# Performance work log

Hardware: AMD Instinct MI355X
Metric: run time of the kernel (lower is better)

Reference implementation:

```python
import jax, jax.numpy as jnp
import numpy as np

N, D, E = 16384, 1024, 65536
HID, H1, NCLS = 512, 8, 2


def _glorot(key, shape):
    fan = shape[0] + shape[-1]
    return jax.random.normal(key, shape, jnp.float32) * np.sqrt(2.0 / fan)


def setup_inputs() -> dict:
    key = jax.random.key(0)
    ks = jax.random.split(key, 12)
    return {
        "x": jax.random.normal(ks[0], (N, D), jnp.float32),
        "edge_index": jax.random.randint(ks[1], (2, E), 0, N, dtype=jnp.int32),
        # layer 1: GATConv((-1,-1), 512, heads=8, concat=True)
        "W1_src": _glorot(ks[2], (D, H1 * HID)),
        "W1_dst": _glorot(ks[3], (D, H1 * HID)),
        "att1_src": _glorot(ks[4], (H1, HID)),
        "att1_dst": _glorot(ks[5], (H1, HID)),
        "b1": jnp.zeros((H1 * HID,), jnp.float32),
        # layer 2: GATConv((-1,-1), 2, heads=1, concat=False)
        "W2_src": _glorot(ks[6], (H1 * HID, NCLS)),
        "W2_dst": _glorot(ks[7], (H1 * HID, NCLS)),
        "att2_src": _glorot(ks[8], (1, NCLS)),
        "att2_dst": _glorot(ks[9], (1, NCLS)),
        "b2": jnp.zeros((NCLS,), jnp.float32),
    }


def gat_layer(x, src, dst, Ws, Wd, a_s, a_d, b, heads, ch, concat):
    n = x.shape[0]
    hs = (x @ Ws).reshape(n, heads, ch)  # source-transformed feats [N,H,C]
    hd = (x @ Wd).reshape(n, heads, ch)  # dest-transformed feats  [N,H,C]
    al_s = jnp.einsum("nhc,hc->nh", hs, a_s)  # [N,H]
    al_d = jnp.einsum("nhc,hc->nh", hd, a_d)
    logits = jax.nn.leaky_relu(al_s[src] + al_d[dst], 0.2)  # [E,H]
    # segment softmax over incoming edges of each destination node
    m = jax.ops.segment_max(logits, dst, num_segments=n)
    m = jnp.where(jnp.isfinite(m), m, 0.0)
    e = jnp.exp(logits - m[dst])
    denom = jax.ops.segment_sum(e, dst, num_segments=n)
    alpha = e / (denom[dst] + 1e-16)  # [E,H]
    msg = hs[src] * alpha[:, :, None]  # [E,H,C]
    out = jax.ops.segment_sum(msg, dst, num_segments=n)  # [N,H,C]
    out = out.reshape(n, heads * ch) if concat else out.mean(axis=1)
    return out + b


def reference(x, edge_index, W1_src, W1_dst, att1_src, att1_dst, b1,
              W2_src, W2_dst, att2_src, att2_dst, b2):
    n = x.shape[0]
    # PyG GATConv adds self-loops by default
    loops = jnp.arange(n, dtype=edge_index.dtype)
    src = jnp.concatenate([edge_index[0], loops])
    dst = jnp.concatenate([edge_index[1], loops])
    h = gat_layer(x, src, dst, W1_src, W1_dst, att1_src, att1_dst, b1,
                  H1, HID, concat=True)  # [N, 4096]
    out = gat_layer(h, src, dst, W2_src, W2_dst, att2_src, att2_dst, b2,
                    1, NCLS, concat=False)  # [N, 2]
    return out
```

## Files before the change

kernel.cpp:

```cpp
#include <hip/hip_runtime.h>
#include <cstdint>
#include <cstddef>

#define DEV __device__ __forceinline__

typedef __attribute__((ext_vector_type(8))) short bf16x8;
typedef __attribute__((ext_vector_type(4))) float f32x4;

constexpr int N_  = 16384;
constexpr int D_  = 1024;
constexpr int E_  = 65536;
constexpr int ET_ = E_ + N_;
constexpr int H_  = 8;
constexpr int C_  = 512;
constexpr int F_  = 4096;
constexpr int KSPLIT = 2;
constexpr int ZS4 = KSPLIT * 48;
constexpr int NVB = 2048;
constexpr int NMB = (N_ / 16) * KSPLIT;

DEV unsigned short f2bf(float f){
  unsigned u = __float_as_uint(f);
  unsigned r = u + 0x7FFFu + ((u >> 16) & 1u);
  return (unsigned short)(r >> 16);
}
DEV float lrelu(float x){ return x >= 0.f ? x : 0.2f * x; }
DEV float waveSum(float v){
  #pragma unroll
  for (int o = 32; o > 0; o >>= 1) v += __shfl_xor(v, o);
  return v;
}
DEV int eSRC(const int* ei, int e){ return e < E_ ? ei[e]      : e - E_; }
DEV int eDST(const int* ei, int e){ return e < E_ ? ei[E_ + e] : e - E_; }

__global__ __launch_bounds__(256) void prep(
    const float* __restrict__ W1s, const float* __restrict__ W1d,
    const float* __restrict__ a1s, const float* __restrict__ a1d,
    const float* __restrict__ W2s, const float* __restrict__ W2d,
    const float* __restrict__ a2d, const float* __restrict__ b1,
    unsigned short* __restrict__ Vb, float* __restrict__ cb){
  int t = threadIdx.x;
  int bx = blockIdx.x;
  if (bx < NVB){
    int id = bx * 4 + (t >> 6);
    int lane = t & 63;
    int d = id >> 3, h = id & 7;
    float a2d0 = a2d[0], a2d1 = a2d[1];
    float sa = 0.f, sb = 0.f, s0 = 0.f, s1 = 0.f, sd = 0.f;
    #pragma unroll
    for (int i = 0; i < C_ / 64; i++){
      int c = i * 64 + lane;
      int gc = h * C_ + c;
      float ws  = W1s[(size_t)d * F_ + gc];
      float wdv = W1d[(size_t)d * F_ + gc];
      sa += ws * a1s[gc]; sb += wdv * a1d[gc];
      float2 w2 = *reinterpret_cast<const float2*>(W2s + (size_t)gc * 2);
      float2 wx = *reinterpret_cast<const float2*>(W2d + (size_t)gc * 2);
      s0 += ws * w2.x; s1 += ws * w2.y;
      sd += ws * (wx.x * a2d0 + wx.y * a2d1);
    }
    sa = waveSum(sa); sb = waveSum(sb);
    s0 = waveSum(s0); s1 = waveSum(s1); sd = waveSum(sd);
    if (lane == 0){
      int kc = d >> 5, ks = (d >> 3) & 3, ii = d & 7;
      auto put = [&](int jj, float v){
        int tt = jj >> 4, j = jj & 15;
        Vb[((size_t)(tt * 32 + kc) * 64 + ks * 16 + j) * 8 + ii] = f2bf(v);
      };
      put(h, sa); put(8 + h, sb); put(16 + h, s0); put(24 + h, s1); put(32 + h, sd);
    }
  } else {
    __shared__ float red[3][4];
    int w = t >> 6, lane = t & 63;
    float a2d0 = a2d[0], a2d1 = a2d[1];
    float p0 = 0.f, p1 = 0.f, pd = 0.f;
    for (int k = t; k < F_; k += 256){
      float b = b1[k];
      float2 w2 = *reinterpret_cast<const float2*>(W2s + (size_t)k * 2);
      float2 wx = *reinterpret_cast<const float2*>(W2d + (size_t)k * 2);
      p0 += b * w2.x; p1 += b * w2.y; pd += b * (wx.x * a2d0 + wx.y * a2d1);
    }
    p0 = waveSum(p0); p1 = waveSum(p1); pd = waveSum(pd);
    if (lane == 0){ red[0][w] = p0; red[1][w] = p1; red[2][w] = pd; }
    __syncthreads();
    if (t == 0){
      cb[0] = red[0][0] + red[0][1] + red[0][2] + red[0][3];
      cb[1] = red[1][0] + red[1][1] + red[1][2] + red[1][3];
      cb[2] = red[2][0] + red[2][1] + red[2][2] + red[2][3];
    }
  }
}

__global__ __launch_bounds__(64) void node_mfma(const float* __restrict__ X,
                                                const unsigned short* __restrict__ Vb,
                                                float* __restrict__ Z4,
                                                uint4* __restrict__ zr, int n16){
  int bx = blockIdx.x;
  int lane = threadIdx.x;
  if (bx >= NMB){
    int i = (bx - NMB) * 64 + lane;
    if (i < n16){ uint4 z = {0u,0u,0u,0u}; zr[i] = z; }
    return;
  }
  int n0 = (bx >> 1) * 16;
  int kh = bx & 1;
  int row = lane & 15, ks = lane >> 4;
  f32x4 ac0 = {0.f,0.f,0.f,0.f}, ac1 = ac0, ac2 = ac0;
  const float* xp = X + (size_t)(n0 + row) * D_ + ks * 8;
  constexpr int KC = 32 / KSPLIT;
  #pragma unroll 2
  for (int kk = 0; kk < KC; kk++){
    int kc = kh * KC + kk;
    float4 xa = *reinterpret_cast<const float4*>(xp + kc * 32);
    float4 xb = *reinterpret_cast<const float4*>(xp + kc * 32 + 4);
    bf16x8 a;
    a[0] = (short)f2bf(xa.x); a[1] = (short)f2bf(xa.y);
    a[2] = (short)f2bf(xa.z); a[3] = (short)f2bf(xa.w);
    a[4] = (short)f2bf(xb.x); a[5] = (short)f2bf(xb.y);
    a[6] = (short)f2bf(xb.z); a[7] = (short)f2bf(xb.w);
    bf16x8 b0 = *reinterpret_cast<const bf16x8*>(&Vb[((size_t)( 0 + kc) * 64 + lane) * 8]);
    bf16x8 b1 = *reinterpret_cast<const bf16x8*>(&Vb[((size_t)(32 + kc) * 64 + lane) * 8]);
    bf16x8 b2 = *reinterpret_cast<const bf16x8*>(&Vb[((size_t)(64 + kc) * 64 + lane) * 8]);
    ac0 = __builtin_amdgcn_mfma_f32_16x16x32_bf16(a, b0, ac0, 0, 0, 0);
    ac1 = __builtin_amdgcn_mfma_f32_16x16x32_bf16(a, b1, ac1, 0, 0, 0);
    ac2 = __builtin_amdgcn_mfma_f32_16x16x32_bf16(a, b2, ac2, 0, 0, 0);
  }
  #pragma unroll
  for (int r = 0; r < 4; r++){
    int n = n0 + ks * 4 + r;
    float* zp = Z4 + (size_t)n * ZS4 + kh * 48;
    zp[ 0 + row] = ac0[r];
    zp[16 + row] = ac1[r];
    zp[32 + row] = ac2[r];
  }
}

__global__ void edge1(const int* __restrict__ ei, const float* __restrict__ Z4,
                      float* __restrict__ den1, float* __restrict__ a0,
                      float* __restrict__ a1, float* __restrict__ ad){
  int t = blockIdx.x * blockDim.x + threadIdx.x;
  if (t >= ET_ * H_) return;
  int e = t >> 3, h = t & 7;
  int s = eSRC(ei, e), d = eDST(ei, e);
  const float* zs = Z4 + (size_t)s * ZS4;
  const float* zd = Z4 + (size_t)d * ZS4;
  float zsh = 0.f, zdh = 0.f, z0 = 0.f, z1 = 0.f, zdd = 0.f;
  #pragma unroll
  for (int k = 0; k < KSPLIT; k++){
    int o = k * 48;
    zsh += zs[o + h];
    zdh += zd[o + 8 + h];
    z0  += zs[o + 16 + h];
    z1  += zs[o + 24 + h];
    zdd += zs[o + 32 + h];
  }
  float ev = expf(lrelu(zsh + zdh));
  int o = d * 8 + h;
  atomicAdd(&den1[o], ev);
  atomicAdd(&a0[o], ev * z0);
  atomicAdd(&a1[o], ev * z1);
  atomicAdd(&ad[o], ev * zdd);
}

__global__ void node_mid(const float* __restrict__ den1, const float* __restrict__ a0,
                         const float* __restrict__ a1, const float* __restrict__ ad,
                         const float* __restrict__ cb, const float* __restrict__ a2s,
                         float4* __restrict__ Pn){
  int n = blockIdx.x * blockDim.x + threadIdx.x;
  if (n >= N_) return;
  float v0 = 0.f, v1 = 0.f, vd = 0.f;
  #pragma unroll
  for (int h = 0; h < 8; h++){
    float inv = 1.f / (den1[n * 8 + h] + 1e-16f);
    v0 += a0[n * 8 + h] * inv;
    v1 += a1[n * 8 + h] * inv;
    vd += ad[n * 8 + h] * inv;
  }
  v0 += cb[0]; v1 += cb[1]; vd += cb[2];
  float4 r;
  r.x = v0 * a2s[0] + v1 * a2s[1];
  r.y = v0; r.z = v1;
  r.w = vd;
  Pn[n] = r;
}

__global__ void edge2(const int* __restrict__ ei, const float4* __restrict__ Pn,
                      float* __restrict__ den2, float* __restrict__ o0,
                      float* __restrict__ o1){
  int e = blockIdx.x * blockDim.x + threadIdx.x;
  if (e >= ET_) return;
  int s = eSRC(ei, e), d = eDST(ei, e);
  float4 ps = Pn[s];
  float ald = Pn[d].w;
  float ev = expf(lrelu(ps.x + ald));
  atomicAdd(&den2[d], ev);
  atomicAdd(&o0[d], ev * ps.y);
  atomicAdd(&o1[d], ev * ps.z);
}

__global__ void node_out(const float* __restrict__ den2, const float* __restrict__ o0,
                         const float* __restrict__ o1, const float* __restrict__ b2,
                         float* __restrict__ out){
  int n = blockIdx.x * blockDim.x + threadIdx.x;
  if (n >= N_) return;
  float inv = 1.f / (den2[n] + 1e-16f);
  out[2 * n]     = o0[n] * inv + b2[0];
  out[2 * n + 1] = o1[n] * inv + b2[1];
}

extern "C" void kernel_launch(void* const* d_in, const int* in_sizes, int n_in,
                              void* d_out, int out_size, void* d_ws, size_t ws_size,
                              hipStream_t stream){
  const float* x   = (const float*)d_in[0];
  const int*   ei  = (const int*)  d_in[1];
  const float* W1s = (const float*)d_in[2];
  const float* W1d = (const float*)d_in[3];
  const float* a1s = (const float*)d_in[4];
  const float* a1d = (const float*)d_in[5];
  const float* b1  = (const float*)d_in[6];
  const float* W2s = (const float*)d_in[7];
  const float* W2d = (const float*)d_in[8];
  const float* a2s = (const float*)d_in[9];
  const float* a2d = (const float*)d_in[10];
  const float* b2  = (const float*)d_in[11];
  float* out = (float*)d_out;

  char* p = (char*)d_ws;
  auto alloc = [&](size_t bytes) -> void* {
    void* r = (void*)p;
    p += (bytes + 255) & ~(size_t)255;
    return r;
  };
  float* Z4 = (float*)alloc((size_t)N_ * ZS4 * 4);
  float* den1  = (float*)alloc((size_t)N_ * H_ * 4);
  float* a0    = (float*)alloc((size_t)N_ * H_ * 4);
  float* a1    = (float*)alloc((size_t)N_ * H_ * 4);
  float* ad    = (float*)alloc((size_t)N_ * H_ * 4);
  float* den2  = (float*)alloc((size_t)N_ * 4);
  float* o0    = (float*)alloc((size_t)N_ * 4);
  float* o1    = (float*)alloc((size_t)N_ * 4);
  unsigned short* Vb = (unsigned short*)alloc((size_t)3 * 32 * 64 * 8 * 2);
  float* cb    = (float*)alloc(256);
  float4* Pn   = (float4*)alloc((size_t)N_ * 16);

  size_t zrBytes = (size_t)((char*)Vb - (char*)den1);
  int n16 = (int)(zrBytes / 16);
  int nzb = (n16 + 63) / 64;

  prep<<<dim3(NVB + 1), dim3(256), 0, stream>>>(W1s, W1d, a1s, a1d, W2s, W2d,
                                                a2d, b1, Vb, cb);
  node_mfma<<<dim3(NMB + nzb), dim3(64), 0, stream>>>(x, Vb, Z4, (uint4*)den1, n16);
  edge1<<<dim3(ET_ * H_ / 256), dim3(256), 0, stream>>>(ei, Z4, den1, a0, a1, ad);
  node_mid<<<dim3(N_ / 256), dim3(256), 0, stream>>>(den1, a0, a1, ad, cb, a2s, Pn);
  edge2<<<dim3(ET_ / 256), dim3(256), 0, stream>>>(ei, Pn, den2, o0, o1);
  node_out<<<dim3(N_ / 256), dim3(256), 0, stream>>>(den2, o0, o1, b2, out);
}
```

Before: 67.19 us.

## Reduce K-split in-block via LDS and interleave edge accumulators per node

The node projection kernel now runs both K halves as two waves in one block and sums them through shared memory, so Z holds a single 48-float row per node instead of two partial rows. The edge kernel then reads each value once rather than summing two partials. The four per-head accumulators (denominator and three weighted sums) are merged into one node-major array of 32 floats, so the atomics for a node land in nearby cache lines. The cost is a block-wide barrier and LDS traffic in the projection kernel, plus fewer, larger blocks.

```diff
diff --git a/kernel.cpp b/kernel.cpp
--- a/kernel.cpp
+++ b/kernel.cpp
@@ -14,10 +14,9 @@
 constexpr int H_  = 8;
 constexpr int C_  = 512;
 constexpr int F_  = 4096;
-constexpr int KSPLIT = 2;
-constexpr int ZS4 = KSPLIT * 48;
+constexpr int ZS_ = 48;
 constexpr int NVB = 2048;
-constexpr int NMB = (N_ / 16) * KSPLIT;
+constexpr int NMB = N_ / 16;
 
 DEV unsigned short f2bf(float f){
   unsigned u = __float_as_uint(f);
@@ -91,26 +90,26 @@
   }
 }
 
-__global__ __launch_bounds__(64) void node_mfma(const float* __restrict__ X,
-                                                const unsigned short* __restrict__ Vb,
-                                                float* __restrict__ Z4,
-                                                uint4* __restrict__ zr, int n16){
+__global__ __launch_bounds__(128) void node_mfma(const float* __restrict__ X,
+                                                 const unsigned short* __restrict__ Vb,
+                                                 float* __restrict__ Z,
+                                                 uint4* __restrict__ zr, int n16){
   int bx = blockIdx.x;
-  int lane = threadIdx.x;
+  int t = threadIdx.x;
   if (bx >= NMB){
-    int i = (bx - NMB) * 64 + lane;
+    int i = (bx - NMB) * 128 + t;
     if (i < n16){ uint4 z = {0u,0u,0u,0u}; zr[i] = z; }
     return;
   }
-  int n0 = (bx >> 1) * 16;
-  int kh = bx & 1;
+  __shared__ float sm[16][52];
+  int kh = t >> 6, lane = t & 63;
+  int n0 = bx * 16;
   int row = lane & 15, ks = lane >> 4;
   f32x4 ac0 = {0.f,0.f,0.f,0.f}, ac1 = ac0, ac2 = ac0;
   const float* xp = X + (size_t)(n0 + row) * D_ + ks * 8;
-  constexpr int KC = 32 / KSPLIT;
   #pragma unroll 2
-  for (int kk = 0; kk < KC; kk++){
-    int kc = kh * KC + kk;
+  for (int kk = 0; kk < 16; kk++){
+    int kc = kh * 16 + kk;
     float4 xa = *reinterpret_cast<const float4*>(xp + kc * 32);
     float4 xb = *reinterpret_cast<const float4*>(xp + kc * 32 + 4);
     bf16x8 a;
@@ -125,56 +124,55 @@
     ac1 = __builtin_amdgcn_mfma_f32_16x16x32_bf16(a, b1, ac1, 0, 0, 0);
     ac2 = __builtin_amdgcn_mfma_f32_16x16x32_bf16(a, b2, ac2, 0, 0, 0);
   }
-  #pragma unroll
-  for (int r = 0; r < 4; r++){
-    int n = n0 + ks * 4 + r;
-    float* zp = Z4 + (size_t)n * ZS4 + kh * 48;
-    zp[ 0 + row] = ac0[r];
-    zp[16 + row] = ac1[r];
-    zp[32 + row] = ac2[r];
-  }
-}
-
-__global__ void edge1(const int* __restrict__ ei, const float* __restrict__ Z4,
-                      float* __restrict__ den1, float* __restrict__ a0,
-                      float* __restrict__ a1, float* __restrict__ ad){
+  if (kh == 1){
+    #pragma unroll
+    for (int r = 0; r < 4; r++){
+      int nl = ks * 4 + r;
+      sm[nl][ 0 + row] = ac0[r];
+      sm[nl][16 + row] = ac1[r];
+      sm[nl][32 + row] = ac2[r];
+    }
+  }
+  __syncthreads();
+  if (kh == 0){
+    #pragma unroll
+    for (int r = 0; r < 4; r++){
+      int nl = ks * 4 + r;
+      float* zp = Z + (size_t)(n0 + nl) * ZS_;
+      zp[ 0 + row] = ac0[r] + sm[nl][ 0 + row];
+      zp[16 + row] = ac1[r] + sm[nl][16 + row];
+      zp[32 + row] = ac2[r] + sm[nl][32 + row];
+    }
+  }
+}
+
+__global__ void edge1(const int* __restrict__ ei, const float* __restrict__ Z,
+                      float* __restrict__ acc){
   int t = blockIdx.x * blockDim.x + threadIdx.x;
   if (t >= ET_ * H_) return;
   int e = t >> 3, h = t & 7;
   int s = eSRC(ei, e), d = eDST(ei, e);
-  const float* zs = Z4 + (size_t)s * ZS4;
-  const float* zd = Z4 + (size_t)d * ZS4;
-  float zsh = 0.f, zdh = 0.f, z0 = 0.f, z1 = 0.f, zdd = 0.f;
-  #pragma unroll
-  for (int k = 0; k < KSPLIT; k++){
-    int o = k * 48;
-    zsh += zs[o + h];
-    zdh += zd[o + 8 + h];
-    z0  += zs[o + 16 + h];
-    z1  += zs[o + 24 + h];
-    zdd += zs[o + 32 + h];
-  }
-  float ev = expf(lrelu(zsh + zdh));
-  int o = d * 8 + h;
-  atomicAdd(&den1[o], ev);
-  atomicAdd(&a0[o], ev * z0);
-  atomicAdd(&a1[o], ev * z1);
-  atomicAdd(&ad[o], ev * zdd);
-}
-
-__global__ void node_mid(const float* __restrict__ den1, const float* __restrict__ a0,
-                         const float* __restrict__ a1, const float* __restrict__ ad,
-                         const float* __restrict__ cb, const float* __restrict__ a2s,
-                         float4* __restrict__ Pn){
+  const float* zs = Z + (size_t)s * ZS_;
+  float ev = expf(lrelu(zs[h] + Z[(size_t)d * ZS_ + 8 + h]));
+  float* ap = acc + (size_t)d * 32 + h;
+  atomicAdd(ap +  0, ev);
+  atomicAdd(ap +  8, ev * zs[16 + h]);
+  atomicAdd(ap + 16, ev * zs[24 + h]);
+  atomicAdd(ap + 24, ev * zs[32 + h]);
+}
+
+__global__ void node_mid(const float* __restrict__ acc, const float* __restrict__ cb,
+                         const float* __restrict__ a2s, float4* __restrict__ Pn){
   int n = blockIdx.x * blockDim.x + threadIdx.x;
   if (n >= N_) return;
+  const float* ap = acc + (size_t)n * 32;
   float v0 = 0.f, v1 = 0.f, vd = 0.f;
   #pragma unroll
   for (int h = 0; h < 8; h++){
-    float inv = 1.f / (den1[n * 8 + h] + 1e-16f);
-    v0 += a0[n * 8 + h] * inv;
-    v1 += a1[n * 8 + h] * inv;
-    vd += ad[n * 8 + h] * inv;
+    float inv = 1.f / (ap[h] + 1e-16f);
+    v0 += ap[ 8 + h] * inv;
+    v1 += ap[16 + h] * inv;
+    vd += ap[24 + h] * inv;
   }
   v0 += cb[0]; v1 += cb[1]; vd += cb[2];
   float4 r;
@@ -231,11 +229,8 @@
     p += (bytes + 255) & ~(size_t)255;
     return r;
   };
-  float* Z4 = (float*)alloc((size_t)N_ * ZS4 * 4);
-  float* den1  = (float*)alloc((size_t)N_ * H_ * 4);
-  float* a0    = (float*)alloc((size_t)N_ * H_ * 4);
-  float* a1    = (float*)alloc((size_t)N_ * H_ * 4);
-  float* ad    = (float*)alloc((size_t)N_ * H_ * 4);
+  float* Z = (float*)alloc((size_t)N_ * ZS_ * 4);
+  float* acc   = (float*)alloc((size_t)N_ * 32 * 4);
   float* den2  = (float*)alloc((size_t)N_ * 4);
   float* o0    = (float*)alloc((size_t)N_ * 4);
   float* o1    = (float*)alloc((size_t)N_ * 4);
@@ -243,15 +238,15 @@
   float* cb    = (float*)alloc(256);
   float4* Pn   = (float4*)alloc((size_t)N_ * 16);
 
-  size_t zrBytes = (size_t)((char*)Vb - (char*)den1);
+  size_t zrBytes = (size_t)((char*)Vb - (char*)acc);
   int n16 = (int)(zrBytes / 16);
-  int nzb = (n16 + 63) / 64;
+  int nzb = (n16 + 127) / 128;
 
   prep<<<dim3(NVB + 1), dim3(256), 0, stream>>>(W1s, W1d, a1s, a1d, W2s, W2d,
                                                 a2d, b1, Vb, cb);
-  node_mfma<<<dim3(NMB + nzb), dim3(64), 0, stream>>>(x, Vb, Z4, (uint4*)den1, n16);
-  edge1<<<dim3(ET_ * H_ / 256), dim3(256), 0, stream>>>(ei, Z4, den1, a0, a1, ad);
-  node_mid<<<dim3(N_ / 256), dim3(256), 0, stream>>>(den1, a0, a1, ad, cb, a2s, Pn);
+  node_mfma<<<dim3(NMB + nzb), dim3(128), 0, stream>>>(x, Vb, Z, (uint4*)acc, n16);
+  edge1<<<dim3(ET_ * H_ / 256), dim3(256), 0, stream>>>(ei, Z, acc);
+  node_mid<<<dim3(N_ / 256), dim3(256), 0, stream>>>(acc, cb, a2s, Pn);
   edge2<<<dim3(ET_ / 256), dim3(256), 0, stream>>>(ei, Pn, den2, o0, o1);
   node_out<<<dim3(N_ / 256), dim3(256), 0, stream>>>(den2, o0, o1, b2, out);
 }
```

Measured after the change: 69.06 us. 1.03x slower.
